# Kernel tuning notes

Hardware: AMD Instinct MI355X
Metric: run time of the kernel (lower is better)

Reference implementation:

```python
import jax, jax.numpy as jnp
import numpy as np

N = 20000          # nodes
E = 320000         # edges (avg degree 16)
D_IN, D1, D2, D_OUT = 256, 512, 256, 64
EPS = 1e-5


def _glorot(key, shape):
    lim = (6.0 / (shape[0] + shape[1])) ** 0.5
    return jax.random.uniform(key, shape, jnp.float32, -lim, lim)


def setup_inputs() -> dict:
    key = jax.random.key(0)
    ks = jax.random.split(key, 8)
    x = jax.random.normal(ks[0], (N, D_IN), jnp.float32)
    edge_index = jax.random.randint(ks[1], (2, E), 0, N, dtype=jnp.int64)
    return {
        "x": x,
        "edge_index": edge_index,
        # SAGEConv 1 (SoftmaxAggregation temperature t1 over inp_dim channels)
        "t1": jnp.ones((1, D_IN), jnp.float32),
        "Wl1": _glorot(ks[2], (D_IN, D1)), "bl1": jnp.zeros((D1,), jnp.float32),
        "Wr1": _glorot(ks[3], (D_IN, D1)),
        "g1": jnp.ones((D1,), jnp.float32), "beta1": jnp.zeros((D1,), jnp.float32),
        # SAGEConv 2
        "t2": jnp.ones((1, D1), jnp.float32),
        "Wl2": _glorot(ks[4], (D1, D2)), "bl2": jnp.zeros((D2,), jnp.float32),
        "Wr2": _glorot(ks[5], (D1, D2)),
        "g2": jnp.ones((D2,), jnp.float32), "beta2": jnp.zeros((D2,), jnp.float32),
        # final linear + LayerNorm
        "Wf": _glorot(ks[6], (D2, D_OUT)), "bf": jnp.zeros((D_OUT,), jnp.float32),
        "gx": jnp.ones((D_OUT,), jnp.float32), "betax": jnp.zeros((D_OUT,), jnp.float32),
    }


def _sage_softmax(x, src, dst, t, Wl, bl, Wr, n):
    """SAGEConv with learnable per-channel SoftmaxAggregation."""
    m = x[src]                                              # [E, C] gathered messages
    a = m * t                                               # scaled logits
    amax = jax.ops.segment_max(a, dst, num_segments=n)      # [N, C]
    e = jnp.exp(a - amax[dst])
    denom = jax.ops.segment_sum(e, dst, num_segments=n)     # [N, C]
    w = e / denom[dst]                                      # segment softmax weights
    agg = jax.ops.segment_sum(m * w, dst, num_segments=n)   # weighted neighbor sum
    return agg @ Wl + bl + x @ Wr


def _graph_ln(x, g, b):
    # PyG LayerNorm mode='graph', batch=None: normalize over ALL nodes & channels
    mu = x.mean()
    std = jnp.sqrt(((x - mu) ** 2).mean())
    return (x - mu) / (std + EPS) * g + b


def _ln(x, g, b):
    mu = x.mean(-1, keepdims=True)
    var = ((x - mu) ** 2).mean(-1, keepdims=True)
    return (x - mu) / jnp.sqrt(var + EPS) * g + b


def reference(x, edge_index, t1, Wl1, bl1, Wr1, g1, beta1,
              t2, Wl2, bl2, Wr2, g2, beta2, Wf, bf, gx, betax):
    src, dst = edge_index[0], edge_index[1]
    h = _sage_softmax(x, src, dst, t1, Wl1, bl1, Wr1, N)
    h = jax.nn.relu(_graph_ln(h, g1, beta1))
    h = _sage_softmax(h, src, dst, t2, Wl2, bl2, Wr2, N)
    h = jax.nn.relu(_graph_ln(h, g2, beta2))
    p = h.mean(0, keepdims=True)                            # global_mean_pool, batch=None -> [1, 256]
    out = _ln(p @ Wf + bf, gx, betax)
    return jax.nn.relu(out)
```

## Files before the change

### kernel.cpp

```cpp
#include <hip/hip_runtime.h>
#include <math.h>

#define NODES 20000
#define MPAD  20096
#define EDGES 320000
#define EPSV  1e-5f
#define LOG2E 1.4426950408889634f

#define PREP_CNT   1250
#define PREP_CAST  5000
#define PREP_TR    512
#define PREP_TOTAL (PREP_CNT + PREP_CAST + PREP_TR + 1)

typedef short bf16x8 __attribute__((ext_vector_type(8)));
typedef float f32x4  __attribute__((ext_vector_type(4)));
typedef float f2     __attribute__((ext_vector_type(2)));

__device__ __forceinline__ unsigned short f2bf(float f) {
    unsigned int u = __float_as_uint(f);
    u = (u + 0x7fffu + ((u >> 16) & 1u)) >> 16;
    return (unsigned short)u;
}
__device__ __forceinline__ float bf2f(unsigned short h) {
    return __uint_as_float(((unsigned int)h) << 16);
}

__device__ __forceinline__ void load_lds16(const unsigned short* g, unsigned short* l) {
    __builtin_amdgcn_global_load_lds(
        (const __attribute__((address_space(1))) unsigned int*)g,
        (__attribute__((address_space(3))) unsigned int*)l, 16, 0, 0);
}

__global__ void k_prep(const int* __restrict__ dst, int* __restrict__ counts,
                       const float* __restrict__ x, unsigned short* __restrict__ xb,
                       const float* __restrict__ Wl1, const float* __restrict__ Wr1,
                       const float* __restrict__ Wl2, const float* __restrict__ Wr2,
                       unsigned short* __restrict__ o1l, unsigned short* __restrict__ o1r,
                       unsigned short* __restrict__ o2l, unsigned short* __restrict__ o2r,
                       float* __restrict__ acc, float* __restrict__ colsum) {
    int b = blockIdx.x;
    int t = threadIdx.x;
    if (b < PREP_CNT) {
        int e = b * 256 + t;
        if (e < EDGES) atomicAdd(&counts[dst[e]], 1);
    } else if (b < PREP_CNT + PREP_CAST) {
        int i = ((b - PREP_CNT) * 256 + t) * 4;
        float4 v = *(const float4*)(x + i);
        xb[i + 0] = f2bf(v.x); xb[i + 1] = f2bf(v.y);
        xb[i + 2] = f2bf(v.z); xb[i + 3] = f2bf(v.w);
    } else if (b < PREP_CNT + PREP_CAST + PREP_TR) {
        __shared__ float tile[32][33];
        int zz = b - PREP_CNT - PREP_CAST;
        int z = zz >> 7;
        int idx = zz & 127;
        const float* W = (z == 0) ? Wl1 : (z == 1) ? Wr1 : (z == 2) ? Wl2 : Wr2;
        unsigned short* Wt = (z == 0) ? o1l : (z == 1) ? o1r : (z == 2) ? o2l : o2r;
        int K = (z < 2) ? 256 : 512, N = (z < 2) ? 512 : 256;
        int nb = N / 32;
        int n0 = (idx % nb) * 32, k0 = (idx / nb) * 32;
        int tx = t & 31, ty = t >> 5;
#pragma unroll
        for (int j = 0; j < 4; j++)
            tile[ty + j * 8][tx] = W[(size_t)(k0 + ty + j * 8) * N + n0 + tx];
        __syncthreads();
#pragma unroll
        for (int j = 0; j < 4; j++)
            Wt[(size_t)(n0 + ty + j * 8) * K + k0 + tx] = f2bf(tile[tx][ty + j * 8]);
    } else {
        if (t < 4) acc[t] = 0.f;
        colsum[t] = 0.f;
    }
}

__global__ void k_scan(const int* __restrict__ counts, int* __restrict__ offs) {
    __shared__ int ssum[256];
    int t = threadIdx.x;
    const int chunk = (NODES + 255) / 256;
    int b = t * chunk, e = b + chunk;
    if (b > NODES) b = NODES;
    if (e > NODES) e = NODES;
    int s = 0;
    for (int i = b; i < e; i++) s += counts[i];
    ssum[t] = s;
    __syncthreads();
    int v = s;
#pragma unroll
    for (int o = 1; o < 256; o <<= 1) {
        int add = (t >= o) ? ssum[t - o] : 0;
        __syncthreads();
        v += add;
        ssum[t] = v;
        __syncthreads();
    }
    int run = v - s;
    if (t == 255) offs[NODES] = v;
    for (int i = b; i < e; i++) { offs[i] = run; run += counts[i]; }
}

__global__ void k_scatter(const int* __restrict__ src, const int* __restrict__ dst,
                          const int* __restrict__ offs, int* __restrict__ cursor,
                          int* __restrict__ csr_src) {
    int e = blockIdx.x * blockDim.x + threadIdx.x;
    if (e < EDGES) {
        int d = dst[e];
        int pos = atomicAdd(&cursor[d], 1);
        csr_src[offs[d] + pos] = src[e];
    }
}

template <int C, int S, int UNR>
__global__ void k_agg(const unsigned short* __restrict__ xb, const float* __restrict__ tt,
                      const int* __restrict__ offs, const int* __restrict__ csr,
                      unsigned short* __restrict__ out) {
    constexpr int CS  = C / S;
    constexpr int VPL = CS / 64;
    constexpr int W   = VPL / 2;
    typedef unsigned int uv __attribute__((ext_vector_type(W)));
    typedef unsigned short usv __attribute__((ext_vector_type(VPL)));
    int waveg = (int)((blockIdx.x * (unsigned)blockDim.x + threadIdx.x) >> 6);
    int lane = threadIdx.x & 63;
    int node = waveg / S;
    int slice = waveg % S;
    if (node >= NODES) return;
    int beg = __builtin_amdgcn_readfirstlane(offs[node]);
    int end = __builtin_amdgcn_readfirstlane(offs[node + 1]);
    int cb = slice * CS + lane * VPL;
    const unsigned short* __restrict__ xcb = xb + cb;
    f2 tl[W], l[W], s[W];
#pragma unroll
    for (int i = 0; i < W; i++) {
        tl[i][0] = tt[cb + 2 * i] * LOG2E;
        tl[i][1] = tt[cb + 2 * i + 1] * LOG2E;
        l[i][0] = 0.f; l[i][1] = 0.f;
        s[i][0] = 0.f; s[i][1] = 0.f;
    }
    int k = beg;
    for (; k + UNR <= end; k += UNR) {
        uv v[UNR];
#pragma unroll
        for (int u = 0; u < UNR; u++) {
            int sn = csr[k + u];
            v[u] = *(const uv*)(xcb + (size_t)sn * C);
        }
#pragma unroll
        for (int u = 0; u < UNR; u++)
#pragma unroll
            for (int i = 0; i < W; i++) {
                unsigned wd = v[u][i];
                f2 xv;
                xv[0] = __uint_as_float(wd << 16);
                xv[1] = __uint_as_float(wd & 0xffff0000u);
                f2 a = xv * tl[i];
                f2 p;
                p[0] = __builtin_amdgcn_exp2f(a[0]);
                p[1] = __builtin_amdgcn_exp2f(a[1]);
                l[i] += p;
                s[i] = __builtin_elementwise_fma(p, xv, s[i]);
            }
    }
    for (; k < end; k++) {
        int sn = csr[k];
        uv vv = *(const uv*)(xcb + (size_t)sn * C);
#pragma unroll
        for (int i = 0; i < W; i++) {
            unsigned wd = vv[i];
            f2 xv;
            xv[0] = __uint_as_float(wd << 16);
            xv[1] = __uint_as_float(wd & 0xffff0000u);
            f2 a = xv * tl[i];
            f2 p;
            p[0] = __builtin_amdgcn_exp2f(a[0]);
            p[1] = __builtin_amdgcn_exp2f(a[1]);
            l[i] += p;
            s[i] = __builtin_elementwise_fma(p, xv, s[i]);
        }
    }
    bool has = end > beg;
    usv o;
#pragma unroll
    for (int i = 0; i < W; i++) {
        o[2 * i]     = f2bf(has ? s[i][0] / l[i][0] : 0.f);
        o[2 * i + 1] = f2bf(has ? s[i][1] / l[i][1] : 0.f);
    }
    *(usv*)(out + (size_t)node * C + cb) = o;
}

template <int K, int NT, int NTILES, int TN>
__global__ __launch_bounds__(256) void k_gemm_mfma(
    const unsigned short* __restrict__ A1, const unsigned short* __restrict__ B1t,
    const unsigned short* __restrict__ A2, const unsigned short* __restrict__ B2t,
    const float* __restrict__ bias, unsigned short* __restrict__ Co, int M,
    float* __restrict__ stat) {
    constexpr int NF = TN / 32;
    __shared__ short As[128 * 32];
    __shared__ short Bs[TN * 32];
    __shared__ float rs[256], rq[256];

    int bx = blockIdx.x;
    int xid = bx & 7, q = bx >> 3;
    int n = q % NTILES, mh = q / NTILES;
    int m = mh * 8 + xid;
    if (m * 128 >= MPAD) return;
    int m0 = m * 128, n0 = n * TN;

    int t = threadIdx.x;
    int wv = t >> 6, lane = t & 63;
    int wm = wv & 1, wn = wv >> 1;
    int lm = lane & 15, quad = lane >> 4;
    int sr = t >> 2;
    int sc8 = (t & 3) * 8;

    f32x4 acc[4][NF] = {};

    for (int ph = 0; ph < 2; ph++) {
        const unsigned short* __restrict__ A  = ph ? A2 : A1;
        const unsigned short* __restrict__ Bt = ph ? B2t : B1t;
        for (int k0 = 0; k0 < K; k0 += 32) {
#pragma unroll
            for (int it = 0; it < 2; it++)
                load_lds16(A + (size_t)(m0 + it * 64 + sr) * K + k0 + sc8,
                           (unsigned short*)&As[it * 2048 + wv * 512]);
#pragma unroll
            for (int it = 0; it < TN / 64; it++)
                load_lds16(Bt + (size_t)(n0 + it * 64 + sr) * K + k0 + sc8,
                           (unsigned short*)&Bs[it * 2048 + wv * 512]);
            __syncthreads();
            bf16x8 af[4], bfr[NF];
#pragma unroll
            for (int i = 0; i < 4; i++)
                af[i] = *(const bf16x8*)&As[(wm * 64 + i * 16 + lm) * 32 + quad * 8];
#pragma unroll
            for (int j = 0; j < NF; j++)
                bfr[j] = *(const bf16x8*)&Bs[(wn * (TN / 2) + j * 16 + lm) * 32 + quad * 8];
#pragma unroll
            for (int mi = 0; mi < 4; mi++)
#pragma unroll
                for (int nj = 0; nj < NF; nj++)
                    acc[mi][nj] = __builtin_amdgcn_mfma_f32_16x16x32_bf16(
                        af[mi], bfr[nj], acc[mi][nj], 0, 0, 0);
            __syncthreads();
        }
    }

    float sum = 0.f, ss = 0.f;
#pragma unroll
    for (int mi = 0; mi < 4; mi++) {
        int rb = m0 + wm * 64 + mi * 16 + quad * 4;
#pragma unroll
        for (int nj = 0; nj < NF; nj++) {
            int col = n0 + wn * (TN / 2) + nj * 16 + lm;
            float bb = bias[col];
#pragma unroll
            for (int rg = 0; rg < 4; rg++) {
                int row = rb + rg;
                if (row < M) {
                    float y = acc[mi][nj][rg] + bb;
                    Co[(size_t)row * NT + col] = f2bf(y);
                    sum += y; ss += y * y;
                }
            }
        }
    }
    rs[t] = sum; rq[t] = ss;
    __syncthreads();
    for (int o = 128; o > 0; o >>= 1) {
        if (t < o) { rs[t] += rs[t + o]; rq[t] += rq[t + o]; }
        __syncthreads();
    }
    if (t == 0) { atomicAdd(&stat[0], rs[0]); atomicAdd(&stat[1], rq[0]); }
}

template <int C>
__global__ void k_ln_relu_b(unsigned short* __restrict__ h, int n,
                            const float* __restrict__ st,
                            const float* __restrict__ g, const float* __restrict__ b) {
    typedef unsigned short us8 __attribute__((ext_vector_type(8)));
    float mu = st[0] / (float)n;
    float var = st[1] / (float)n - mu * mu;
    var = var < 0.f ? 0.f : var;
    float inv = 1.0f / (sqrtf(var) + EPSV);
    int i8 = (blockIdx.x * blockDim.x + threadIdx.x) * 8;
    if (i8 >= n) return;
    int c = i8 & (C - 1);
    us8 v = *(const us8*)(h + i8);
    us8 o;
#pragma unroll
    for (int j = 0; j < 8; j++) {
        float y = (bf2f(v[j]) - mu) * inv * g[c + j] + b[c + j];
        o[j] = f2bf(fmaxf(y, 0.f));
    }
    *(us8*)(h + i8) = o;
}

__global__ void k_ln_colsum(const unsigned short* __restrict__ h, int n,
                            const float* __restrict__ st,
                            const float* __restrict__ g, const float* __restrict__ b,
                            float* __restrict__ colsum) {
    float mu = st[0] / (float)n;
    float var = st[1] / (float)n - mu * mu;
    var = var < 0.f ? 0.f : var;
    float inv = 1.0f / (sqrtf(var) + EPSV);
    int t = threadIdx.x;
    float gv = g[t], bv = b[t];
    float local = 0.f;
    int stride = gridDim.x * blockDim.x;
    for (int i = blockIdx.x * blockDim.x + t; i < n; i += stride) {
        float y = (bf2f(h[i]) - mu) * inv * gv + bv;
        local += fmaxf(y, 0.f);
    }
    atomicAdd(&colsum[t], local);
}

__global__ void k_final(const float* __restrict__ colsum, const float* __restrict__ Wf,
                        const float* __restrict__ bf, const float* __restrict__ gx,
                        const float* __restrict__ bx, float* __restrict__ out) {
    __shared__ float p[256];
    int t = threadIdx.x;
    p[t] = colsum[t] * (1.0f / (float)NODES);
    __syncthreads();
    if (t < 64) {
        float acc = bf[t];
        for (int c = 0; c < 256; c++) acc = fmaf(p[c], Wf[c * 64 + t], acc);
        float sum = acc;
        for (int o = 32; o > 0; o >>= 1) sum += __shfl_xor(sum, o);
        float mu = sum * (1.0f / 64.0f);
        float d = acc - mu;
        float vs = d * d;
        for (int o = 32; o > 0; o >>= 1) vs += __shfl_xor(vs, o);
        float var = vs * (1.0f / 64.0f);
        float y = d * rsqrtf(var + EPSV) * gx[t] + bx[t];
        out[t] = fmaxf(y, 0.f);
    }
}

extern "C" void kernel_launch(void* const* d_in, const int* in_sizes, int n_in,
                              void* d_out, int out_size, void* d_ws, size_t ws_size,
                              hipStream_t stream) {
    const float* x   = (const float*)d_in[0];
    const int*   ei  = (const int*)d_in[1];
    const float* t1  = (const float*)d_in[2];
    const float* Wl1 = (const float*)d_in[3];
    const float* bl1 = (const float*)d_in[4];
    const float* Wr1 = (const float*)d_in[5];
    const float* g1  = (const float*)d_in[6];
    const float* be1 = (const float*)d_in[7];
    const float* t2  = (const float*)d_in[8];
    const float* Wl2 = (const float*)d_in[9];
    const float* bl2 = (const float*)d_in[10];
    const float* Wr2 = (const float*)d_in[11];
    const float* g2  = (const float*)d_in[12];
    const float* be2 = (const float*)d_in[13];
    const float* Wf  = (const float*)d_in[14];
    const float* bf  = (const float*)d_in[15];
    const float* gx  = (const float*)d_in[16];
    const float* bx  = (const float*)d_in[17];
    float* out = (float*)d_out;

    char* ws = (char*)d_ws;
    size_t off = 0;
    auto alloc = [&](size_t bytes) { size_t o = off; off = (off + bytes + 511) & ~511ull; return o; };
    size_t o_counts = alloc((size_t)NODES * 4);
    size_t o_cursor = alloc((size_t)NODES * 4);
    size_t zero_bytes = off;
    size_t o_acc    = alloc(4 * 4);
    size_t o_colsum = alloc(256 * 4);
    size_t o_offs = alloc((size_t)(NODES + 1) * 4);
    size_t o_csrc = alloc((size_t)EDGES * 4);
    size_t o_w1l  = alloc((size_t)512 * 256 * 2);
    size_t o_w1r  = alloc((size_t)512 * 256 * 2);
    size_t o_w2l  = alloc((size_t)256 * 512 * 2);
    size_t o_w2r  = alloc((size_t)256 * 512 * 2);
    size_t o_bufX = alloc((size_t)MPAD * 256 * 2);
    size_t o_agg  = alloc((size_t)MPAD * 512 * 2);
    size_t o_h1   = alloc((size_t)(MPAD + 512) * 512 * 2);

    int*   counts = (int*)(ws + o_counts);
    int*   cursor = (int*)(ws + o_cursor);
    float* acc    = (float*)(ws + o_acc);
    float* colsum = (float*)(ws + o_colsum);
    int*   offs   = (int*)(ws + o_offs);
    int*   csrc   = (int*)(ws + o_csrc);
    unsigned short* w1lt = (unsigned short*)(ws + o_w1l);
    unsigned short* w1rt = (unsigned short*)(ws + o_w1r);
    unsigned short* w2lt = (unsigned short*)(ws + o_w2l);
    unsigned short* w2rt = (unsigned short*)(ws + o_w2r);
    unsigned short* xb   = (unsigned short*)(ws + o_bufX);
    unsigned short* h2p  = (unsigned short*)(ws + o_bufX);
    unsigned short* aggb = (unsigned short*)(ws + o_agg);
    unsigned short* h1   = (unsigned short*)(ws + o_h1);

    const int* src = ei;
    const int* dst = ei + EDGES;

    hipMemsetAsync(ws, 0, zero_bytes, stream);

    k_prep<<<PREP_TOTAL, 256, 0, stream>>>(dst, counts, x, xb,
                                           Wl1, Wr1, Wl2, Wr2,
                                           w1lt, w1rt, w2lt, w2rt,
                                           acc, colsum);
    k_scan<<<1, 256, 0, stream>>>(counts, offs);
    k_scatter<<<(EDGES + 255) / 256, 256, 0, stream>>>(src, dst, offs, cursor, csrc);

    k_agg<256, 2, 8><<<(NODES * 2 + 3) / 4, 256, 0, stream>>>(xb, t1, offs, csrc, aggb);
    k_gemm_mfma<256, 512, 4, 128><<<8 * 4 * 20, 256, 0, stream>>>(
        aggb, w1lt, xb, w1rt, bl1, h1, NODES, acc);
    k_ln_relu_b<512><<<NODES * 512 / 8 / 256, 256, 0, stream>>>(h1, NODES * 512, acc, g1, be1);

    k_agg<512, 2, 4><<<(NODES * 2 + 3) / 4, 256, 0, stream>>>(h1, t2, offs, csrc, aggb);
    k_gemm_mfma<512, 256, 2, 128><<<8 * 2 * 20, 256, 0, stream>>>(
        aggb, w2lt, h1, w2rt, bl2, h2p, NODES, acc + 2);

    k_ln_colsum<<<1024, 256, 0, stream>>>(h2p, NODES * 256, acc + 2, g2, be2, colsum);
    k_final<<<1, 256, 0, stream>>>(colsum, Wf, bf, gx, bx, out);
}
```

Measured before the change: 349.1 us.

## Double-buffer GEMM LDS tiles, widen scan to 1024 threads, parallelize final matvec

The MFMA GEMM now keeps two LDS buffers and issues the async global-to-LDS load for the next K step before computing the current one. This is meant to overlap memory latency with MFMA work and drops one barrier per step. The single-block scan now uses 1024 threads with per-thread register chunks, which shortens the serial per-thread loop. The final matvec is split across all four waves and reduced through shared memory. The cost is twice the LDS per GEMM block, which may lower occupancy.

Result: faster. 333.9 us (-4.4%).

```diff
diff --git a/kernel.cpp b/kernel.cpp
--- a/kernel.cpp
+++ b/kernel.cpp
@@ -72,29 +72,38 @@
     }
 }
 
-__global__ void k_scan(const int* __restrict__ counts, int* __restrict__ offs) {
-    __shared__ int ssum[256];
+#define SCAN_PN 20
+
+__global__ __launch_bounds__(1024) void k_scan(const int* __restrict__ counts,
+                                               int* __restrict__ offs) {
+    __shared__ int sm[1024];
     int t = threadIdx.x;
-    const int chunk = (NODES + 255) / 256;
-    int b = t * chunk, e = b + chunk;
-    if (b > NODES) b = NODES;
-    if (e > NODES) e = NODES;
+    int i0 = t * SCAN_PN;
+    int c[SCAN_PN];
     int s = 0;
-    for (int i = b; i < e; i++) s += counts[i];
-    ssum[t] = s;
+#pragma unroll
+    for (int j = 0; j < SCAN_PN; j++) {
+        int i = i0 + j;
+        c[j] = (i < NODES) ? counts[i] : 0;
+        s += c[j];
+    }
+    sm[t] = s;
     __syncthreads();
     int v = s;
-#pragma unroll
-    for (int o = 1; o < 256; o <<= 1) {
-        int add = (t >= o) ? ssum[t - o] : 0;
+    for (int o = 1; o < 1024; o <<= 1) {
+        int add = (t >= o) ? sm[t - o] : 0;
         __syncthreads();
         v += add;
-        ssum[t] = v;
+        sm[t] = v;
         __syncthreads();
     }
     int run = v - s;
-    if (t == 255) offs[NODES] = v;
-    for (int i = b; i < e; i++) { offs[i] = run; run += counts[i]; }
+    if (t == 1023) offs[NODES] = v;
+#pragma unroll
+    for (int j = 0; j < SCAN_PN; j++) {
+        int i = i0 + j;
+        if (i < NODES) { offs[i] = run; run += c[j]; }
+    }
 }
 
 __global__ void k_scatter(const int* __restrict__ src, const int* __restrict__ dst,
@@ -192,8 +201,10 @@
     const float* __restrict__ bias, unsigned short* __restrict__ Co, int M,
     float* __restrict__ stat) {
     constexpr int NF = TN / 32;
-    __shared__ short As[128 * 32];
-    __shared__ short Bs[TN * 32];
+    constexpr int H = K / 32;
+    constexpr int NSTEP = 2 * H;
+    __shared__ short As[2][128 * 32];
+    __shared__ short Bs[2][TN * 32];
     __shared__ float rs[256], rq[256];
 
     int bx = blockIdx.x;
@@ -212,34 +223,39 @@
 
     f32x4 acc[4][NF] = {};
 
-    for (int ph = 0; ph < 2; ph++) {
-        const unsigned short* __restrict__ A  = ph ? A2 : A1;
-        const unsigned short* __restrict__ Bt = ph ? B2t : B1t;
-        for (int k0 = 0; k0 < K; k0 += 32) {
-#pragma unroll
-            for (int it = 0; it < 2; it++)
-                load_lds16(A + (size_t)(m0 + it * 64 + sr) * K + k0 + sc8,
-                           (unsigned short*)&As[it * 2048 + wv * 512]);
-#pragma unroll
-            for (int it = 0; it < TN / 64; it++)
-                load_lds16(Bt + (size_t)(n0 + it * 64 + sr) * K + k0 + sc8,
-                           (unsigned short*)&Bs[it * 2048 + wv * 512]);
-            __syncthreads();
-            bf16x8 af[4], bfr[NF];
-#pragma unroll
-            for (int i = 0; i < 4; i++)
-                af[i] = *(const bf16x8*)&As[(wm * 64 + i * 16 + lm) * 32 + quad * 8];
-#pragma unroll
-            for (int j = 0; j < NF; j++)
-                bfr[j] = *(const bf16x8*)&Bs[(wn * (TN / 2) + j * 16 + lm) * 32 + quad * 8];
-#pragma unroll
-            for (int mi = 0; mi < 4; mi++)
-#pragma unroll
-                for (int nj = 0; nj < NF; nj++)
-                    acc[mi][nj] = __builtin_amdgcn_mfma_f32_16x16x32_bf16(
-                        af[mi], bfr[nj], acc[mi][nj], 0, 0, 0);
-            __syncthreads();
-        }
+    auto stage = [&](int s, int buf) {
+        const unsigned short* __restrict__ A  = (s < H) ? A1 : A2;
+        const unsigned short* __restrict__ Bt = (s < H) ? B1t : B2t;
+        int k0 = (s & (H - 1)) * 32;
+#pragma unroll
+        for (int it = 0; it < 2; it++)
+            load_lds16(A + (size_t)(m0 + it * 64 + sr) * K + k0 + sc8,
+                       (unsigned short*)&As[buf][it * 2048 + wv * 512]);
+#pragma unroll
+        for (int it = 0; it < TN / 64; it++)
+            load_lds16(Bt + (size_t)(n0 + it * 64 + sr) * K + k0 + sc8,
+                       (unsigned short*)&Bs[buf][it * 2048 + wv * 512]);
+    };
+
+    stage(0, 0);
+    __syncthreads();
+    for (int s = 0; s < NSTEP; s++) {
+        int cur = s & 1;
+        if (s + 1 < NSTEP) stage(s + 1, cur ^ 1);
+        bf16x8 af[4], bfr[NF];
+#pragma unroll
+        for (int i = 0; i < 4; i++)
+            af[i] = *(const bf16x8*)&As[cur][(wm * 64 + i * 16 + lm) * 32 + quad * 8];
+#pragma unroll
+        for (int j = 0; j < NF; j++)
+            bfr[j] = *(const bf16x8*)&Bs[cur][(wn * (TN / 2) + j * 16 + lm) * 32 + quad * 8];
+#pragma unroll
+        for (int mi = 0; mi < 4; mi++)
+#pragma unroll
+            for (int nj = 0; nj < NF; nj++)
+                acc[mi][nj] = __builtin_amdgcn_mfma_f32_16x16x32_bf16(
+                    af[mi], bfr[nj], acc[mi][nj], 0, 0, 0);
+        __syncthreads();
     }
 
     float sum = 0.f, ss = 0.f;
@@ -315,18 +331,27 @@
                         const float* __restrict__ bf, const float* __restrict__ gx,
                         const float* __restrict__ bx, float* __restrict__ out) {
     __shared__ float p[256];
+    __shared__ float red[4][64];
     int t = threadIdx.x;
     p[t] = colsum[t] * (1.0f / (float)NODES);
     __syncthreads();
+    int kg = t >> 6, o = t & 63;
+    float a = 0.f;
+#pragma unroll
+    for (int j = 0; j < 64; j++) {
+        int c = kg + j * 4;
+        a = fmaf(p[c], Wf[c * 64 + o], a);
+    }
+    red[kg][o] = a;
+    __syncthreads();
     if (t < 64) {
-        float acc = bf[t];
-        for (int c = 0; c < 256; c++) acc = fmaf(p[c], Wf[c * 64 + t], acc);
+        float acc = bf[t] + red[0][t] + red[1][t] + red[2][t] + red[3][t];
         float sum = acc;
-        for (int o = 32; o > 0; o >>= 1) sum += __shfl_xor(sum, o);
+        for (int w = 32; w > 0; w >>= 1) sum += __shfl_xor(sum, w);
         float mu = sum * (1.0f / 64.0f);
         float d = acc - mu;
         float vs = d * d;
-        for (int o = 32; o > 0; o >>= 1) vs += __shfl_xor(vs, o);
+        for (int w = 32; w > 0; w >>= 1) vs += __shfl_xor(vs, w);
         float var = vs * (1.0f / 64.0f);
         float y = d * rsqrtf(var + EPSV) * gx[t] + bx[t];
         out[t] = fmaxf(y, 0.f);
@@ -398,7 +423,7 @@
                                            Wl1, Wr1, Wl2, Wr2,
                                            w1lt, w1rt, w2lt, w2rt,
                                            acc, colsum);
-    k_scan<<<1, 256, 0, stream>>>(counts, offs);
+    k_scan<<<1, 1024, 0, stream>>>(counts, offs);
     k_scatter<<<(EDGES + 255) / 256, 256, 0, stream>>>(src, dst, offs, cursor, csrc);
 
     k_agg<256, 2, 8><<<(NODES * 2 + 3) / 4, 256, 0, stream>>>(xb, t1, offs, csrc, aggb);
```
